# Optimization experiments

Measured on AMD Instinct MI355X. Metric: run time of the kernel, lower is better.

## Reference

```python
import jax, jax.numpy as jnp
import numpy as np

N_LEAVES = 32768
DEPTH = 16               # tree levels, leaves at level 0
N_NODES = 2 * N_LEAVES - 1
H = 256                  # h_size
X = 300                  # x_size
FEAT = 1024              # image feature_size
R = 49                   # image regions
VOCAB = 30000
CLASSES = 5


def setup_inputs() -> dict:
    ks = jax.random.split(jax.random.key(0), 10)
    wordid = jax.random.randint(ks[0], (N_NODES,), 0, VOCAB, dtype=jnp.int32)
    # leaves carry word tokens (mask=1), internal nodes don't (mask=0)
    mask = jnp.concatenate([jnp.ones(N_LEAVES, jnp.int32),
                            jnp.zeros(N_NODES - N_LEAVES, jnp.int32)])
    image = jax.random.normal(ks[1], (R, FEAT), dtype=jnp.float32)
    h0 = jnp.zeros((N_NODES, H), jnp.float32)
    c0 = jnp.zeros((N_NODES, H), jnp.float32)
    s = lambda k, shp, fan: jax.random.normal(k, shp, dtype=jnp.float32) * (1.0 / np.sqrt(fan))
    emb = s(ks[2], (VOCAB, X), X)
    attn_w_in = s(ks[3], (X, FEAT), FEAT)            # Attention.linear_in (no bias)
    attn_w_out = s(ks[4], (X, X + FEAT), X + FEAT)   # Attention.linear_out
    attn_b_out = jnp.zeros((X,), jnp.float32)
    w_iou = s(ks[5], (3 * H, X), X)                  # cell.W_iou (no bias)
    u_iou = s(ks[6], (3 * H, 2 * H), 2 * H)          # cell.U_iou (no bias)
    b_iou = jnp.zeros((1, 3 * H), jnp.float32)
    u_f_w = s(ks[7], (2 * H, 2 * H), 2 * H)          # cell.U_f
    u_f_b = jnp.zeros((2 * H,), jnp.float32)
    lin_w = s(ks[8], (CLASSES, H), H)                # final classifier
    lin_b = jnp.zeros((CLASSES,), jnp.float32)
    return dict(wordid=wordid, mask=mask, image=image, h0=h0, c0=c0, emb=emb,
                attn_w_in=attn_w_in, attn_w_out=attn_w_out, attn_b_out=attn_b_out,
                w_iou=w_iou, u_iou=u_iou, b_iou=b_iou, u_f_w=u_f_w, u_f_b=u_f_b,
                lin_w=lin_w, lin_b=lin_b)


def _forward(wordid, mask, image, h0, c0, emb, attn_w_in, attn_w_out, attn_b_out,
             w_iou, u_iou, b_iou, u_f_w, u_f_b, lin_w, lin_b):
    # --- embedding + attention over image regions ---
    embeds = emb[wordid * mask]                                  # [N, X]
    img_in = image @ attn_w_in.T                                 # [R, X]
    atten = jax.nn.softmax(embeds @ img_in.T, axis=1)            # [N, R]
    context = atten @ image                                      # [N, FEAT]
    sent = jnp.tanh(jnp.concatenate([context, embeds], axis=1) @ attn_w_out.T + attn_b_out)
    iou_x = (sent @ w_iou.T) * mask[:, None].astype(sent.dtype)  # [N, 3H] (dropout p=0 -> identity)

    def apply_node(iou, c_in):
        i, o, u = jnp.split(iou + b_iou, 3, axis=1)
        c_new = jax.nn.sigmoid(i) * jnp.tanh(u) + c_in
        return jax.nn.sigmoid(o) * jnp.tanh(c_new), c_new

    # --- leaves: no mailbox, apply_node with initial c ---
    h_leaf, c_leaf = apply_node(iou_x[:N_LEAVES], c0[:N_LEAVES])
    h = h0.at[:N_LEAVES].set(h_leaf)
    c = c0.at[:N_LEAVES].set(c_leaf)

    # --- topological propagation, one dense level at a time ---
    off_prev, sz, off = 0, N_LEAVES, N_LEAVES
    for _ in range(DEPTH - 1):
        sz_new = sz // 2
        h_cat = jax.lax.dynamic_slice_in_dim(h, off_prev, sz).reshape(sz_new, 2 * H)
        c_ch = jax.lax.dynamic_slice_in_dim(c, off_prev, sz).reshape(sz_new, 2, H)
        f = jax.nn.sigmoid(h_cat @ u_f_w.T + u_f_b).reshape(sz_new, 2, H)
        c_red = jnp.sum(f * c_ch, axis=1)                        # [sz_new, H]
        iou = h_cat @ u_iou.T                                    # reduce_func overwrites node iou
        h_new, c_new = apply_node(iou, c_red)
        h = h.at[off:off + sz_new].set(h_new)
        c = c.at[off:off + sz_new].set(c_new)
        off_prev, sz, off = off, sz_new, off + sz_new

    return h @ lin_w.T + lin_b                                   # [N, CLASSES]


def reference(wordid, mask, image, h0, c0, emb, attn_w_in, attn_w_out, attn_b_out,
              w_iou, u_iou, b_iou, u_f_w, u_f_b, lin_w, lin_b):
    return _forward(wordid, mask, image, h0, c0, emb, attn_w_in, attn_w_out, attn_b_out,
                    w_iou, u_iou, b_iou, u_f_w, u_f_b, lin_w, lin_b)
```

## Files before the change

### kernel.cpp

```cpp
#include <hip/hip_runtime.h>
#include <hip/hip_bf16.h>
#include <math.h>

#define N_LEAVES 32768
#define N_NODES  65535
#define DEPTH    16
#define H        256
#define XS       300
#define FEAT     1024
#define RR       49
#define CLASSES  5

#define XP 320
#define CATW 384

typedef __attribute__((ext_vector_type(8))) short bf16x8;
typedef __attribute__((ext_vector_type(4))) float f32x4;

__device__ __forceinline__ ushort f2bf(float v) {
    __hip_bfloat16 h = __float2bfloat16(v);
    return *reinterpret_cast<ushort*>(&h);
}
__device__ __forceinline__ float bf2f(ushort u) {
    __hip_bfloat16 h; *reinterpret_cast<ushort*>(&h) = u;
    return __bfloat162float(h);
}

__device__ __forceinline__ float fsig(float x) {
    float e = __builtin_amdgcn_exp2f(-1.44269504f * x);
    return __builtin_amdgcn_rcpf(1.0f + e);
}
__device__ __forceinline__ float ftanh(float x) {
    float xx = fmaxf(x, -20.0f);
    float e = __builtin_amdgcn_exp2f(-2.88539008f * xx);
    return (1.0f - e) * __builtin_amdgcn_rcpf(1.0f + e);
}
__device__ __forceinline__ float fexp(float x) {
    return __builtin_amdgcn_exp2f(1.44269504f * x);
}

__device__ __forceinline__ void swz_mj(int& mblk, int& jg) {
    int lid = blockIdx.y * gridDim.x + blockIdx.x;
    int mcount = gridDim.y, njg = gridDim.x;
    if ((mcount & 7) == 0) {
        int xcd = lid & 7, q = lid >> 3;
        jg = q % njg;
        mblk = xcd * (mcount >> 3) + q / njg;
    } else { mblk = blockIdx.y; jg = blockIdx.x; }
}

__device__ __forceinline__ ushort* lds_at(ushort* base, int row, int kbyte) {
    int off = row * 128 + kbyte;
    off ^= ((row & 7) << 4);
    return (ushort*)((char*)base + off);
}

__device__ __forceinline__ void gll16(const void* g, void* l) {
    __builtin_amdgcn_global_load_lds(
        (const __attribute__((address_space(1))) unsigned int*)g,
        (__attribute__((address_space(3))) unsigned int*)l, 16, 0, 0);
}

__device__ __forceinline__ void issue_tileA(const ushort* A, long lda, long m0, long mmax,
                                            int k0, ushort* buf, int R, int w, int lane)
{
    const int insts = R >> 5;
#pragma unroll
    for (int q = 0; q < 4; ++q) {
        if (q >= insts) break;
        int dest = (w * insts + q) * 1024;
        int row = (dest >> 7) + (lane >> 3);
        int kb = ((lane & 7) << 4) ^ ((row & 7) << 4);
        long am = m0 + row; if (am > mmax) am = mmax;
        gll16((const char*)(A + am * lda + k0) + kb, (char*)buf + dest);
    }
}

__global__ __launch_bounds__(256)
void k_sent(const ushort* __restrict__ A, const ushort* __restrict__ Wf,
            const float* __restrict__ bias, ushort* __restrict__ Cbf)
{
    __shared__ ushort At[2][128 * 64];
    const int tid = threadIdx.x;
    const int l = tid & 63;
    const int w = tid >> 6;
    const int wr = w >> 1, wc = w & 1;
    int mblk, nb; swz_mj(mblk, nb);
    const long m0 = (long)mblk * 128;
    const ushort* wb = Wf + (long)(nb * 2 + wc) * 6 * 8 * 512 + l * 8;

    bf16x8 wreg[2][4];
    f32x4 acc[4][4] = {};

    auto loadW = [&](int t) {
        const ushort* wt = wb + (long)t * 8 * 512;
#pragma unroll
        for (int kk = 0; kk < 2; ++kk)
#pragma unroll
            for (int j = 0; j < 4; ++j)
                wreg[kk][j] = *(const bf16x8*)(wt + (long)(kk * 4 + j) * 512);
    };

    issue_tileA(A, CATW, m0, N_LEAVES - 1, 0, At[0], 128, w, l);
    loadW(0);
    __syncthreads();
    for (int t = 0; t < 6; ++t) {
        ushort* Ab = At[t & 1];
#pragma unroll
        for (int kk = 0; kk < 2; ++kk) {
            bf16x8 af[4];
#pragma unroll
            for (int i = 0; i < 4; ++i)
                af[i] = *(const bf16x8*)lds_at(Ab, wr * 64 + i * 16 + (l & 15), kk * 64 + (l >> 4) * 16);
#pragma unroll
            for (int j = 0; j < 4; ++j)
#pragma unroll
                for (int i = 0; i < 4; ++i)
                    acc[i][j] = __builtin_amdgcn_mfma_f32_16x16x32_bf16(af[i], wreg[kk][j], acc[i][j], 0, 0, 0);
        }
        if (t + 1 < 6) {
            issue_tileA(A, CATW, m0, N_LEAVES - 1, (t + 1) * 64, At[(t + 1) & 1], 128, w, l);
            loadW(t + 1);
        }
        __syncthreads();
    }
#pragma unroll
    for (int i = 0; i < 4; ++i)
#pragma unroll
        for (int j = 0; j < 4; ++j)
#pragma unroll
            for (int r = 0; r < 4; ++r) {
                long m = m0 + wr * 64 + i * 16 + (l >> 4) * 4 + r;
                long n = (long)nb * 128 + wc * 64 + j * 16 + (l & 15);
                if (n < XS)
                    Cbf[m * XP + n] = f2bf(ftanh(acc[i][j][r] + bias[n]));
            }
}

__global__ __launch_bounds__(256)
void k_attn(const float* __restrict__ emb, const int* __restrict__ wid,
            const ushort* __restrict__ img, ushort* __restrict__ cat)
{
    __shared__ ushort At[128 * 64];
    __shared__ ushort Bt[64 * 64];
    const int tid = threadIdx.x;
    const int l = tid & 63;
    const int w = tid >> 6;
    const long m0 = (long)blockIdx.x * 128;
    const int srow = tid >> 3, skg = tid & 7;

    int wrd[4];
#pragma unroll
    for (int q = 0; q < 4; ++q) wrd[q] = wid[m0 + q * 32 + srow];

    float av[4][8];
    bf16x8 breg[2];
    f32x4 acc[2][4] = {};

    auto loadAB = [&](int t) {
        int c = t * 64 + skg * 8;
#pragma unroll
        for (int q = 0; q < 4; ++q) {
            const float* er = emb + (long)wrd[q] * XS;
            if (c + 8 <= XS) {
                float4 a = *(const float4*)(er + c);
                float4 b = *(const float4*)(er + c + 4);
                av[q][0] = a.x; av[q][1] = a.y; av[q][2] = a.z; av[q][3] = a.w;
                av[q][4] = b.x; av[q][5] = b.y; av[q][6] = b.z; av[q][7] = b.w;
            } else {
#pragma unroll
                for (int u = 0; u < 8; ++u) av[q][u] = (c + u < XS) ? er[c + u] : 0.f;
            }
        }
#pragma unroll
        for (int q = 0; q < 2; ++q)
            breg[q] = *(const bf16x8*)(img + (long)(q * 32 + srow) * XP + t * 64 + skg * 8);
    };
    auto writeAB = [&](int t) {
        int c = t * 64 + skg * 8;
#pragma unroll
        for (int q = 0; q < 4; ++q) {
            int row = q * 32 + srow;
            bf16x8 pk;
#pragma unroll
            for (int u = 0; u < 8; ++u) pk[u] = (short)f2bf(av[q][u]);
            *(bf16x8*)lds_at(At, row, skg * 16) = pk;
            *(bf16x8*)(cat + (m0 + row) * CATW + 64 + c) = pk;
        }
#pragma unroll
        for (int q = 0; q < 2; ++q)
            *(bf16x8*)lds_at(Bt, q * 32 + srow, skg * 16) = breg[q];
    };

    loadAB(0);
    writeAB(0);
    for (int t = 0; t < 5; ++t) {
        __syncthreads();
        if (t + 1 < 5) loadAB(t + 1);
#pragma unroll
        for (int kk = 0; kk < 2; ++kk) {
            bf16x8 af[2], bg[4];
#pragma unroll
            for (int i = 0; i < 2; ++i)
                af[i] = *(const bf16x8*)lds_at(At, w * 32 + i * 16 + (l & 15), kk * 64 + (l >> 4) * 16);
#pragma unroll
            for (int j = 0; j < 4; ++j)
                bg[j] = *(const bf16x8*)lds_at(Bt, j * 16 + (l & 15), kk * 64 + (l >> 4) * 16);
#pragma unroll
            for (int i = 0; i < 2; ++i)
#pragma unroll
                for (int j = 0; j < 4; ++j)
                    acc[i][j] = __builtin_amdgcn_mfma_f32_16x16x32_bf16(af[i], bg[j], acc[i][j], 0, 0, 0);
        }
        if (t + 1 < 5) {
            __syncthreads();
            writeAB(t + 1);
        }
    }
#pragma unroll
    for (int i = 0; i < 2; ++i)
#pragma unroll
        for (int r = 0; r < 4; ++r) {
            long m = m0 + w * 32 + i * 16 + (l >> 4) * 4 + r;
            float v[4]; float mx = -1e30f;
#pragma unroll
            for (int j = 0; j < 4; ++j) {
                int n = j * 16 + (l & 15);
                v[j] = (n < RR) ? acc[i][j][r] : -1e30f;
                mx = fmaxf(mx, v[j]);
            }
#pragma unroll
            for (int sh = 1; sh < 16; sh <<= 1) mx = fmaxf(mx, __shfl_xor(mx, sh));
            float e[4], s = 0.f;
#pragma unroll
            for (int j = 0; j < 4; ++j) { e[j] = fexp(v[j] - mx); s += e[j]; }
#pragma unroll
            for (int sh = 1; sh < 16; sh <<= 1) s += __shfl_xor(s, sh);
            float inv = __builtin_amdgcn_rcpf(s);
#pragma unroll
            for (int j = 0; j < 4; ++j)
                cat[m * CATW + j * 16 + (l & 15)] = f2bf(e[j] * inv);
        }
}

__global__ __launch_bounds__(256)
void k_leaf_fused(const ushort* __restrict__ A, const ushort* __restrict__ Wf,
                  const float* __restrict__ b_iou,
                  ushort* __restrict__ h, ushort* __restrict__ c)
{
    __shared__ ushort At[2][128 * 64];
    const int tid = threadIdx.x;
    const int l = tid & 63;
    const int w = tid >> 6;
    const int wr = w >> 1, wc = w & 1;
    int mblk, jg; swz_mj(mblk, jg);
    const long m0 = (long)mblk * 128;
    const ushort* wb = Wf + (long)(jg * 2 + wc) * 5 * 12 * 512 + l * 8;

    bf16x8 wreg[2][3][2];
    f32x4 acc[3][4][2] = {};

    auto loadW = [&](int t) {
        const ushort* wt = wb + (long)t * 12 * 512;
#pragma unroll
        for (int kk = 0; kk < 2; ++kk)
#pragma unroll
            for (int g = 0; g < 3; ++g)
#pragma unroll
                for (int j = 0; j < 2; ++j)
                    wreg[kk][g][j] = *(const bf16x8*)(wt + (long)((kk * 3 + g) * 2 + j) * 512);
    };

    issue_tileA(A, XP, m0, N_LEAVES - 1, 0, At[0], 128, w, l);
    loadW(0);
    __syncthreads();
    for (int t = 0; t < 5; ++t) {
        ushort* Ab = At[t & 1];
#pragma unroll
        for (int kk = 0; kk < 2; ++kk) {
            bf16x8 af[4];
#pragma unroll
            for (int i = 0; i < 4; ++i)
                af[i] = *(const bf16x8*)lds_at(Ab, wr * 64 + i * 16 + (l & 15), kk * 64 + (l >> 4) * 16);
#pragma unroll
            for (int g = 0; g < 3; ++g)
#pragma unroll
                for (int j = 0; j < 2; ++j)
#pragma unroll
                    for (int i = 0; i < 4; ++i)
                        acc[g][i][j] = __builtin_amdgcn_mfma_f32_16x16x32_bf16(af[i], wreg[kk][g][j], acc[g][i][j], 0, 0, 0);
        }
        if (t + 1 < 5) {
            issue_tileA(A, XP, m0, N_LEAVES - 1, (t + 1) * 64, At[(t + 1) & 1], 128, w, l);
            loadW(t + 1);
        }
        __syncthreads();
    }
#pragma unroll
    for (int i = 0; i < 4; ++i)
#pragma unroll
        for (int j = 0; j < 2; ++j) {
            int jglob = jg * 64 + wc * 32 + j * 16 + (l & 15);
            float bi = b_iou[jglob], bu = b_iou[512 + jglob], bo = b_iou[256 + jglob];
#pragma unroll
            for (int r = 0; r < 4; ++r) {
                long m = m0 + wr * 64 + i * 16 + (l >> 4) * 4 + r;
                float cn = fsig(acc[0][i][j][r] + bi) * ftanh(acc[1][i][j][r] + bu);
                c[m * H + jglob] = f2bf(cn);
                h[m * H + jglob] = f2bf(fsig(acc[2][i][j][r] + bo) * ftanh(cn));
            }
        }
}

__global__ __launch_bounds__(256)
void k_tree_fused(const ushort* __restrict__ A, const ushort* __restrict__ Wf,
                  const float* __restrict__ u_f_b, const float* __restrict__ b_iou,
                  const ushort* __restrict__ csrc,
                  ushort* __restrict__ hdst, ushort* __restrict__ cdst, int sz_new)
{
    __shared__ ushort At[2][64 * 64];
    const int tid = threadIdx.x;
    const int l = tid & 63;
    const int w = tid >> 6;
    const int wr = w >> 1, wc = w & 1;
    int mblk, jg; swz_mj(mblk, jg);
    const long m0 = (long)mblk * 64;
    const ushort* wb = Wf + (long)(jg * 2 + wc) * 8 * 20 * 512 + l * 8;

    bf16x8 wreg[2][5][2];
    f32x4 acc[5][2][2] = {};

    auto loadW = [&](int t) {
        const ushort* wt = wb + (long)t * 20 * 512;
#pragma unroll
        for (int kk = 0; kk < 2; ++kk)
#pragma unroll
            for (int g = 0; g < 5; ++g)
#pragma unroll
                for (int j = 0; j < 2; ++j)
                    wreg[kk][g][j] = *(const bf16x8*)(wt + (long)((kk * 5 + g) * 2 + j) * 512);
    };

    issue_tileA(A, 512, m0, sz_new - 1, 0, At[0], 64, w, l);
    loadW(0);
    __syncthreads();
    for (int t = 0; t < 8; ++t) {
        ushort* Ab = At[t & 1];
#pragma unroll
        for (int kk = 0; kk < 2; ++kk) {
            bf16x8 af[2];
#pragma unroll
            for (int i = 0; i < 2; ++i)
                af[i] = *(const bf16x8*)lds_at(Ab, wr * 32 + i * 16 + (l & 15), kk * 64 + (l >> 4) * 16);
#pragma unroll
            for (int g = 0; g < 5; ++g)
#pragma unroll
                for (int j = 0; j < 2; ++j)
#pragma unroll
                    for (int i = 0; i < 2; ++i)
                        acc[g][i][j] = __builtin_amdgcn_mfma_f32_16x16x32_bf16(af[i], wreg[kk][g][j], acc[g][i][j], 0, 0, 0);
        }
        if (t + 1 < 8) {
            issue_tileA(A, 512, m0, sz_new - 1, (t + 1) * 64, At[(t + 1) & 1], 64, w, l);
            loadW(t + 1);
        }
        __syncthreads();
    }
#pragma unroll
    for (int i = 0; i < 2; ++i)
#pragma unroll
        for (int j = 0; j < 2; ++j) {
            int jglob = jg * 64 + wc * 32 + j * 16 + (l & 15);
            float bf0 = u_f_b[jglob], bf1 = u_f_b[256 + jglob];
            float bi = b_iou[jglob], bu = b_iou[512 + jglob], bo = b_iou[256 + jglob];
#pragma unroll
            for (int r = 0; r < 4; ++r) {
                long m = m0 + wr * 32 + i * 16 + (l >> 4) * 4 + r;
                if (m < sz_new) {
                    float cl = bf2f(csrc[(2 * m) * H + jglob]);
                    float cr = bf2f(csrc[(2 * m + 1) * H + jglob]);
                    float S = fsig(acc[0][i][j][r] + bf0) * cl
                            + fsig(acc[1][i][j][r] + bf1) * cr;
                    float cn = fsig(acc[2][i][j][r] + bi) * ftanh(acc[3][i][j][r] + bu) + S;
                    cdst[m * H + jglob] = f2bf(cn);
                    hdst[m * H + jglob] = f2bf(fsig(acc[4][i][j][r] + bo) * ftanh(cn));
                }
            }
        }
}

__global__ __launch_bounds__(256)
void k_prep(const float* __restrict__ image, const float* __restrict__ w_in,
            const float* __restrict__ w_out, ushort* __restrict__ img_bf,
            ushort* __restrict__ wcat)
{
    const int wave = (blockIdx.x * 256 + threadIdx.x) >> 6;
    const int lane = threadIdx.x & 63;
    const int half = RR * XS;
    if (wave >= 2 * half) return;
    const float* wr; const float* ir; ushort* outp;
    if (wave < half) {
        int r = wave / XS, x = wave % XS;
        ir = image + (long)r * FEAT;
        wr = w_in + (long)x * FEAT;
        outp = img_bf + (long)r * XP + x;
    } else {
        int w2 = wave - half;
        int x = w2 / RR, r = w2 % RR;
        ir = image + (long)r * FEAT;
        wr = w_out + (long)x * (FEAT + XS);
        outp = wcat + (long)x * CATW + r;
    }
    float s = 0.f;
#pragma unroll
    for (int u = 0; u < FEAT / 64; ++u) {
        int f = lane + u * 64;
        s = fmaf(ir[f], wr[f], s);
    }
#pragma unroll
    for (int sh = 32; sh; sh >>= 1) s += __shfl_xor(s, sh);
    if (lane == 0) *outp = f2bf(s);
}

__global__ __launch_bounds__(256)
void k_cvt(ushort* __restrict__ dst, long dld, long doff,
           const float* __restrict__ src, long sld, long soff,
           int rows, int cols)
{
    long idx = (long)blockIdx.x * 256 + threadIdx.x;
    if (idx >= (long)rows * cols) return;
    int r = (int)(idx / cols), c = (int)(idx % cols);
    dst[r * dld + doff + c] = f2bf(src[r * sld + soff + c]);
}

__global__ __launch_bounds__(256)
void k_bld_wcatf(ushort* __restrict__ dst, const ushort* __restrict__ wcat)
{
    long idx = (long)blockIdx.x * 256 + threadIdx.x;
    if (idx >= 147456) return;
    int u = idx & 7; long r = idx >> 3;
    int l = r & 63; r >>= 6;
    int j = r & 3; r >>= 2;
    int kk = r & 1; r >>= 1;
    int t = (int)(r % 6); r /= 6;
    int wc = r & 1; r >>= 1;
    int nb = (int)r;
    int row = nb * 128 + wc * 64 + j * 16 + (l & 15);
    int col = t * 64 + kk * 32 + (l >> 4) * 8 + u;
    dst[idx] = wcat[(long)row * CATW + col];
}

__global__ __launch_bounds__(256)
void k_bld_w3f(ushort* __restrict__ dst, const float* __restrict__ w_iou)
{
    long idx = (long)blockIdx.x * 256 + threadIdx.x;
    if (idx >= 245760) return;
    int u = idx & 7; long r = idx >> 3;
    int l = r & 63; r >>= 6;
    int j = r & 1; r >>= 1;
    int g = (int)(r % 3); r /= 3;
    int kk = r & 1; r >>= 1;
    int t = (int)(r % 5); r /= 5;
    int wc = r & 1; r >>= 1;
    int jg = (int)r;
    int row = jg * 64 + wc * 32 + j * 16 + (l & 15);
    int col = t * 64 + kk * 32 + (l >> 4) * 8 + u;
    int srow = (g == 0) ? row : (g == 1) ? 512 + row : 256 + row;
    dst[idx] = (col < XS) ? f2bf(w_iou[(long)srow * XS + col]) : 0;
}

__global__ __launch_bounds__(256)
void k_bld_w5f(ushort* __restrict__ dst, const float* __restrict__ u_f_w,
               const float* __restrict__ u_iou)
{
    long idx = (long)blockIdx.x * 256 + threadIdx.x;
    if (idx >= 655360) return;
    int u = idx & 7; long r = idx >> 3;
    int l = r & 63; r >>= 6;
    int j = r & 1; r >>= 1;
    int g = (int)(r % 5); r /= 5;
    int kk = r & 1; r >>= 1;
    int t = (int)(r & 7); r >>= 3;
    int wc = r & 1; r >>= 1;
    int jg = (int)r;
    int row = jg * 64 + wc * 32 + j * 16 + (l & 15);
    int col = t * 64 + kk * 32 + (l >> 4) * 8 + u;
    const float* src;
    if (g == 0)      src = u_f_w + (long)row * 512;
    else if (g == 1) src = u_f_w + (long)(256 + row) * 512;
    else if (g == 2) src = u_iou + (long)row * 512;
    else if (g == 3) src = u_iou + (long)(512 + row) * 512;
    else             src = u_iou + (long)(256 + row) * 512;
    dst[idx] = f2bf(src[col]);
}

__global__ __launch_bounds__(256)
void k_classify(const ushort* __restrict__ h, const float* __restrict__ lin_w,
                const float* __restrict__ lin_b, float* __restrict__ out, int n_rows)
{
    const int node = (int)((blockIdx.x * 256 + threadIdx.x) >> 6);
    const int lane = threadIdx.x & 63;
    if (node >= n_rows) return;
    const ushort* hr = h + (long)node * H;
    float p[CLASSES] = {0.f};
#pragma unroll
    for (int u = 0; u < H / 64; ++u) {
        int j = lane + u * 64;
        float hv = bf2f(hr[j]);
#pragma unroll
        for (int cc = 0; cc < CLASSES; ++cc)
            p[cc] = fmaf(hv, lin_w[cc * H + j], p[cc]);
    }
#pragma unroll
    for (int cc = 0; cc < CLASSES; ++cc)
#pragma unroll
        for (int sh = 32; sh; sh >>= 1) p[cc] += __shfl_xor(p[cc], sh);
    if (lane == 0) {
#pragma unroll
        for (int cc = 0; cc < CLASSES; ++cc)
            out[(long)node * CLASSES + cc] = p[cc] + lin_b[cc];
    }
}

extern "C" void kernel_launch(void* const* d_in, const int* in_sizes, int n_in,
                              void* d_out, int out_size, void* d_ws, size_t ws_size,
                              hipStream_t stream)
{
    const int*   wordid     = (const int*)  d_in[0];
    const float* image      = (const float*)d_in[2];
    const float* emb        = (const float*)d_in[5];
    const float* attn_w_in  = (const float*)d_in[6];
    const float* attn_w_out = (const float*)d_in[7];
    const float* attn_b_out = (const float*)d_in[8];
    const float* w_iou      = (const float*)d_in[9];
    const float* u_iou      = (const float*)d_in[10];
    const float* b_iou      = (const float*)d_in[11];
    const float* u_f_w      = (const float*)d_in[12];
    const float* u_f_b      = (const float*)d_in[13];
    const float* lin_w      = (const float*)d_in[14];
    const float* lin_b      = (const float*)d_in[15];
    float* out = (float*)d_out;

    char* p = (char*)d_ws;
    auto alloc = [&](size_t bytes) { char* r = p; p += (bytes + 255) & ~255UL; return r; };
    ushort* cat     = (ushort*)alloc((size_t)N_LEAVES * CATW * 2);
    ushort* sentbf  = (ushort*)alloc((size_t)N_LEAVES * XP * 2);
    ushort* hall    = (ushort*)alloc((size_t)65536 * H * 2);
    ushort* cA      = (ushort*)alloc((size_t)N_LEAVES * H * 2);
    ushort* cB      = (ushort*)alloc((size_t)(N_LEAVES/2) * H * 2);
    ushort* img_bf  = (ushort*)alloc((size_t)64 * XP * 2);
    ushort* wcat    = (ushort*)alloc((size_t)CATW * CATW * 2);
    ushort* wcatf   = (ushort*)alloc((size_t)147456 * 2);
    ushort* w3f     = (ushort*)alloc((size_t)245760 * 2);
    ushort* w5f     = (ushort*)alloc((size_t)655360 * 2);
    (void)ws_size;

    hipMemsetAsync(img_bf, 0, (size_t)64 * XP * 2, stream);
    hipMemsetAsync(wcat,   0, (size_t)CATW * CATW * 2, stream);
    {
        int waves = 2 * RR * XS;
        k_prep<<<(waves * 64 + 255) / 256, 256, 0, stream>>>(image, attn_w_in,
                                                             attn_w_out, img_bf, wcat);
    }
    k_cvt<<<((long)XS * XS + 255) / 256, 256, 0, stream>>>(
        wcat, CATW, 64, attn_w_out, FEAT + XS, FEAT, XS, XS);
    k_bld_wcatf<<<(147456 + 255) / 256, 256, 0, stream>>>(wcatf, wcat);
    k_bld_w3f<<<(245760 + 255) / 256, 256, 0, stream>>>(w3f, w_iou);
    k_bld_w5f<<<(655360 + 255) / 256, 256, 0, stream>>>(w5f, u_f_w, u_iou);

    k_attn<<<N_LEAVES / 128, 256, 0, stream>>>(emb, wordid, img_bf, cat);
    k_sent<<<dim3(3, N_LEAVES / 128), 256, 0, stream>>>(cat, wcatf, attn_b_out, sentbf);
    k_leaf_fused<<<dim3(4, N_LEAVES / 128), 256, 0, stream>>>(
        sentbf, w3f, b_iou, hall, cA);

    ushort* csrc = cA; ushort* cdst = cB;
    int node_off = N_LEAVES;
    int sz = N_LEAVES;
    int off_prev = 0;
    for (int lvl = 0; lvl < DEPTH - 1; ++lvl) {
        int sz_new = sz / 2;
        k_tree_fused<<<dim3(4, (sz_new + 63) / 64), 256, 0, stream>>>(
            hall + (long)off_prev * H, w5f, u_f_b, b_iou, csrc,
            hall + (long)node_off * H, cdst, sz_new);
        off_prev = node_off;
        node_off += sz_new;
        ushort* t = csrc; csrc = cdst; cdst = t;
        sz = sz_new;
    }

    k_classify<<<((long)N_NODES * 64 + 255) / 256, 256, 0, stream>>>(
        hall, lin_w, lin_b, out, N_NODES);
}
```

Before: 349.0 us.

## Triple-buffer A tiles and split waves along N in MFMA GEMM kernels

Three GEMM kernels (sentence projection, leaf cell, internal-node cell) now use a three-stage LDS ring for A tiles, issued two steps ahead, and double-buffered weight registers. Each block now needs only one barrier per k-step. The wave layout changes from a 2x2 M/N grid to four waves that each cover the full M tile and a quarter of N, and the weight pre-packing kernels are rewritten to match. The goal is to hide global-load latency and cut synchronisation. The cost is more LDS, more A-fragment reads from LDS per wave, and higher register pressure.

```diff
diff --git a/kernel.cpp b/kernel.cpp
--- a/kernel.cpp
+++ b/kernel.cpp
@@ -39,6 +39,9 @@
     return __builtin_amdgcn_exp2f(1.44269504f * x);
 }
 
+#define SPIN() __builtin_amdgcn_sched_barrier(0)
+#define SBAR() { __builtin_amdgcn_s_barrier(); __builtin_amdgcn_sched_barrier(0); }
+
 __device__ __forceinline__ void swz_mj(int& mblk, int& jg) {
     int lid = blockIdx.y * gridDim.x + blockIdx.x;
     int mcount = gridDim.y, njg = gridDim.x;
@@ -80,61 +83,64 @@
 void k_sent(const ushort* __restrict__ A, const ushort* __restrict__ Wf,
             const float* __restrict__ bias, ushort* __restrict__ Cbf)
 {
-    __shared__ ushort At[2][128 * 64];
+    __shared__ ushort At[3][128 * 64];
     const int tid = threadIdx.x;
     const int l = tid & 63;
     const int w = tid >> 6;
-    const int wr = w >> 1, wc = w & 1;
     int mblk, nb; swz_mj(mblk, nb);
     const long m0 = (long)mblk * 128;
-    const ushort* wb = Wf + (long)(nb * 2 + wc) * 6 * 8 * 512 + l * 8;
-
-    bf16x8 wreg[2][4];
-    f32x4 acc[4][4] = {};
-
-    auto loadW = [&](int t) {
-        const ushort* wt = wb + (long)t * 8 * 512;
+    const ushort* wb = Wf + (size_t)(nb * 4 + w) * 24 * 512 + l * 8;
+
+    bf16x8 wreg[2][2][2];
+    f32x4 acc[2][8] = {};
+
+    auto loadW = [&](int t, int buf) {
+        const ushort* wt = wb + (long)t * 4 * 512;
 #pragma unroll
         for (int kk = 0; kk < 2; ++kk)
 #pragma unroll
-            for (int j = 0; j < 4; ++j)
-                wreg[kk][j] = *(const bf16x8*)(wt + (long)(kk * 4 + j) * 512);
+            for (int j = 0; j < 2; ++j)
+                wreg[buf][kk][j] = *(const bf16x8*)(wt + (long)(kk * 2 + j) * 512);
     };
 
     issue_tileA(A, CATW, m0, N_LEAVES - 1, 0, At[0], 128, w, l);
-    loadW(0);
     __syncthreads();
+    issue_tileA(A, CATW, m0, N_LEAVES - 1, 64, At[1], 128, w, l);
+    SPIN();
+    loadW(0, 0);
+#pragma unroll
     for (int t = 0; t < 6; ++t) {
-        ushort* Ab = At[t & 1];
+        if (t + 2 < 6) issue_tileA(A, CATW, m0, N_LEAVES - 1, (t + 2) * 64, At[(t + 2) % 3], 128, w, l);
+        SPIN();
+        if (t + 1 < 6) loadW(t + 1, (t + 1) & 1);
+        ushort* Ab = At[t % 3];
 #pragma unroll
         for (int kk = 0; kk < 2; ++kk) {
-            bf16x8 af[4];
-#pragma unroll
-            for (int i = 0; i < 4; ++i)
-                af[i] = *(const bf16x8*)lds_at(Ab, wr * 64 + i * 16 + (l & 15), kk * 64 + (l >> 4) * 16);
-#pragma unroll
-            for (int j = 0; j < 4; ++j)
-#pragma unroll
-                for (int i = 0; i < 4; ++i)
-                    acc[i][j] = __builtin_amdgcn_mfma_f32_16x16x32_bf16(af[i], wreg[kk][j], acc[i][j], 0, 0, 0);
-        }
-        if (t + 1 < 6) {
-            issue_tileA(A, CATW, m0, N_LEAVES - 1, (t + 1) * 64, At[(t + 1) & 1], 128, w, l);
-            loadW(t + 1);
-        }
-        __syncthreads();
-    }
-#pragma unroll
-    for (int i = 0; i < 4; ++i)
-#pragma unroll
-        for (int j = 0; j < 4; ++j)
+            bf16x8 af[8];
+#pragma unroll
+            for (int i = 0; i < 8; ++i)
+                af[i] = *(const bf16x8*)lds_at(Ab, i * 16 + (l & 15), kk * 64 + (l >> 4) * 16);
+#pragma unroll
+            for (int j = 0; j < 2; ++j)
+#pragma unroll
+                for (int i = 0; i < 8; ++i)
+                    acc[j][i] = __builtin_amdgcn_mfma_f32_16x16x32_bf16(af[i], wreg[t & 1][kk][j], acc[j][i], 0, 0, 0);
+        }
+        if (t + 1 < 6) SBAR();
+    }
+#pragma unroll
+    for (int j = 0; j < 2; ++j) {
+        long n = (long)nb * 128 + w * 32 + j * 16 + (l & 15);
+        if (n >= XS) continue;
+        float bn = bias[n];
+#pragma unroll
+        for (int i = 0; i < 8; ++i)
 #pragma unroll
             for (int r = 0; r < 4; ++r) {
-                long m = m0 + wr * 64 + i * 16 + (l >> 4) * 4 + r;
-                long n = (long)nb * 128 + wc * 64 + j * 16 + (l & 15);
-                if (n < XS)
-                    Cbf[m * XP + n] = f2bf(ftanh(acc[i][j][r] + bias[n]));
+                long m = m0 + i * 16 + (l >> 4) * 4 + r;
+                Cbf[m * XP + n] = f2bf(ftanh(acc[j][i][r] + bn));
             }
+    }
 }
 
 __global__ __launch_bounds__(256)
@@ -248,68 +254,64 @@
                   const float* __restrict__ b_iou,
                   ushort* __restrict__ h, ushort* __restrict__ c)
 {
-    __shared__ ushort At[2][128 * 64];
+    __shared__ ushort At[3][128 * 64];
     const int tid = threadIdx.x;
     const int l = tid & 63;
     const int w = tid >> 6;
-    const int wr = w >> 1, wc = w & 1;
     int mblk, jg; swz_mj(mblk, jg);
     const long m0 = (long)mblk * 128;
-    const ushort* wb = Wf + (long)(jg * 2 + wc) * 5 * 12 * 512 + l * 8;
-
-    bf16x8 wreg[2][3][2];
-    f32x4 acc[3][4][2] = {};
-
-    auto loadW = [&](int t) {
-        const ushort* wt = wb + (long)t * 12 * 512;
+    const ushort* wb = Wf + (size_t)(jg * 4 + w) * 30 * 512 + l * 8;
+
+    bf16x8 wreg[2][2][3];
+    f32x4 acc[3][8] = {};
+
+    auto loadW = [&](int t, int buf) {
+        const ushort* wt = wb + (long)t * 6 * 512;
 #pragma unroll
         for (int kk = 0; kk < 2; ++kk)
 #pragma unroll
             for (int g = 0; g < 3; ++g)
-#pragma unroll
-                for (int j = 0; j < 2; ++j)
-                    wreg[kk][g][j] = *(const bf16x8*)(wt + (long)((kk * 3 + g) * 2 + j) * 512);
+                wreg[buf][kk][g] = *(const bf16x8*)(wt + (long)(kk * 3 + g) * 512);
     };
 
     issue_tileA(A, XP, m0, N_LEAVES - 1, 0, At[0], 128, w, l);
-    loadW(0);
     __syncthreads();
+    issue_tileA(A, XP, m0, N_LEAVES - 1, 64, At[1], 128, w, l);
+    SPIN();
+    loadW(0, 0);
+#pragma unroll
     for (int t = 0; t < 5; ++t) {
-        ushort* Ab = At[t & 1];
+        if (t + 2 < 5) issue_tileA(A, XP, m0, N_LEAVES - 1, (t + 2) * 64, At[(t + 2) % 3], 128, w, l);
+        SPIN();
+        if (t + 1 < 5) loadW(t + 1, (t + 1) & 1);
+        ushort* Ab = At[t % 3];
 #pragma unroll
         for (int kk = 0; kk < 2; ++kk) {
-            bf16x8 af[4];
-#pragma unroll
-            for (int i = 0; i < 4; ++i)
-                af[i] = *(const bf16x8*)lds_at(Ab, wr * 64 + i * 16 + (l & 15), kk * 64 + (l >> 4) * 16);
+            bf16x8 af[8];
+#pragma unroll
+            for (int i = 0; i < 8; ++i)
+                af[i] = *(const bf16x8*)lds_at(Ab, i * 16 + (l & 15), kk * 64 + (l >> 4) * 16);
 #pragma unroll
             for (int g = 0; g < 3; ++g)
 #pragma unroll
-                for (int j = 0; j < 2; ++j)
-#pragma unroll
-                    for (int i = 0; i < 4; ++i)
-                        acc[g][i][j] = __builtin_amdgcn_mfma_f32_16x16x32_bf16(af[i], wreg[kk][g][j], acc[g][i][j], 0, 0, 0);
-        }
-        if (t + 1 < 5) {
-            issue_tileA(A, XP, m0, N_LEAVES - 1, (t + 1) * 64, At[(t + 1) & 1], 128, w, l);
-            loadW(t + 1);
-        }
-        __syncthreads();
-    }
-#pragma unroll
-    for (int i = 0; i < 4; ++i)
-#pragma unroll
-        for (int j = 0; j < 2; ++j) {
-            int jglob = jg * 64 + wc * 32 + j * 16 + (l & 15);
-            float bi = b_iou[jglob], bu = b_iou[512 + jglob], bo = b_iou[256 + jglob];
+                for (int i = 0; i < 8; ++i)
+                    acc[g][i] = __builtin_amdgcn_mfma_f32_16x16x32_bf16(af[i], wreg[t & 1][kk][g], acc[g][i], 0, 0, 0);
+        }
+        if (t + 1 < 5) SBAR();
+    }
+    {
+        int jglob = jg * 64 + w * 16 + (l & 15);
+        float bi = b_iou[jglob], bu = b_iou[512 + jglob], bo = b_iou[256 + jglob];
+#pragma unroll
+        for (int i = 0; i < 8; ++i)
 #pragma unroll
             for (int r = 0; r < 4; ++r) {
-                long m = m0 + wr * 64 + i * 16 + (l >> 4) * 4 + r;
-                float cn = fsig(acc[0][i][j][r] + bi) * ftanh(acc[1][i][j][r] + bu);
+                long m = m0 + i * 16 + (l >> 4) * 4 + r;
+                float cn = fsig(acc[0][i][r] + bi) * ftanh(acc[1][i][r] + bu);
                 c[m * H + jglob] = f2bf(cn);
-                h[m * H + jglob] = f2bf(fsig(acc[2][i][j][r] + bo) * ftanh(cn));
+                h[m * H + jglob] = f2bf(fsig(acc[2][i][r] + bo) * ftanh(cn));
             }
-        }
+    }
 }
 
 __global__ __launch_bounds__(256)
@@ -318,75 +320,71 @@
                   const ushort* __restrict__ csrc,
                   ushort* __restrict__ hdst, ushort* __restrict__ cdst, int sz_new)
 {
-    __shared__ ushort At[2][64 * 64];
+    __shared__ ushort At[3][64 * 64];
     const int tid = threadIdx.x;
     const int l = tid & 63;
     const int w = tid >> 6;
-    const int wr = w >> 1, wc = w & 1;
     int mblk, jg; swz_mj(mblk, jg);
     const long m0 = (long)mblk * 64;
-    const ushort* wb = Wf + (long)(jg * 2 + wc) * 8 * 20 * 512 + l * 8;
-
-    bf16x8 wreg[2][5][2];
-    f32x4 acc[5][2][2] = {};
-
-    auto loadW = [&](int t) {
-        const ushort* wt = wb + (long)t * 20 * 512;
+    const ushort* wb = Wf + (size_t)(jg * 4 + w) * 80 * 512 + l * 8;
+
+    bf16x8 wreg[2][2][5];
+    f32x4 acc[5][4] = {};
+
+    auto loadW = [&](int t, int buf) {
+        const ushort* wt = wb + (long)t * 10 * 512;
 #pragma unroll
         for (int kk = 0; kk < 2; ++kk)
 #pragma unroll
             for (int g = 0; g < 5; ++g)
-#pragma unroll
-                for (int j = 0; j < 2; ++j)
-                    wreg[kk][g][j] = *(const bf16x8*)(wt + (long)((kk * 5 + g) * 2 + j) * 512);
+                wreg[buf][kk][g] = *(const bf16x8*)(wt + (long)(kk * 5 + g) * 512);
     };
 
     issue_tileA(A, 512, m0, sz_new - 1, 0, At[0], 64, w, l);
-    loadW(0);
     __syncthreads();
+    issue_tileA(A, 512, m0, sz_new - 1, 64, At[1], 64, w, l);
+    SPIN();
+    loadW(0, 0);
+#pragma unroll
     for (int t = 0; t < 8; ++t) {
-        ushort* Ab = At[t & 1];
+        if (t + 2 < 8) issue_tileA(A, 512, m0, sz_new - 1, (t + 2) * 64, At[(t + 2) % 3], 64, w, l);
+        SPIN();
+        if (t + 1 < 8) loadW(t + 1, (t + 1) & 1);
+        ushort* Ab = At[t % 3];
 #pragma unroll
         for (int kk = 0; kk < 2; ++kk) {
-            bf16x8 af[2];
-#pragma unroll
-            for (int i = 0; i < 2; ++i)
-                af[i] = *(const bf16x8*)lds_at(Ab, wr * 32 + i * 16 + (l & 15), kk * 64 + (l >> 4) * 16);
+            bf16x8 af[4];
+#pragma unroll
+            for (int i = 0; i < 4; ++i)
+                af[i] = *(const bf16x8*)lds_at(Ab, i * 16 + (l & 15), kk * 64 + (l >> 4) * 16);
 #pragma unroll
             for (int g = 0; g < 5; ++g)
 #pragma unroll
-                for (int j = 0; j < 2; ++j)
-#pragma unroll
-                    for (int i = 0; i < 2; ++i)
-                        acc[g][i][j] = __builtin_amdgcn_mfma_f32_16x16x32_bf16(af[i], wreg[kk][g][j], acc[g][i][j], 0, 0, 0);
-        }
-        if (t + 1 < 8) {
-            issue_tileA(A, 512, m0, sz_new - 1, (t + 1) * 64, At[(t + 1) & 1], 64, w, l);
-            loadW(t + 1);
-        }
-        __syncthreads();
-    }
-#pragma unroll
-    for (int i = 0; i < 2; ++i)
-#pragma unroll
-        for (int j = 0; j < 2; ++j) {
-            int jglob = jg * 64 + wc * 32 + j * 16 + (l & 15);
-            float bf0 = u_f_b[jglob], bf1 = u_f_b[256 + jglob];
-            float bi = b_iou[jglob], bu = b_iou[512 + jglob], bo = b_iou[256 + jglob];
+                for (int i = 0; i < 4; ++i)
+                    acc[g][i] = __builtin_amdgcn_mfma_f32_16x16x32_bf16(af[i], wreg[t & 1][kk][g], acc[g][i], 0, 0, 0);
+        }
+        if (t + 1 < 8) SBAR();
+    }
+    {
+        int jglob = jg * 64 + w * 16 + (l & 15);
+        float bf0 = u_f_b[jglob], bf1 = u_f_b[256 + jglob];
+        float bi = b_iou[jglob], bu = b_iou[512 + jglob], bo = b_iou[256 + jglob];
+#pragma unroll
+        for (int i = 0; i < 4; ++i)
 #pragma unroll
             for (int r = 0; r < 4; ++r) {
-                long m = m0 + wr * 32 + i * 16 + (l >> 4) * 4 + r;
+                long m = m0 + i * 16 + (l >> 4) * 4 + r;
                 if (m < sz_new) {
                     float cl = bf2f(csrc[(2 * m) * H + jglob]);
                     float cr = bf2f(csrc[(2 * m + 1) * H + jglob]);
-                    float S = fsig(acc[0][i][j][r] + bf0) * cl
-                            + fsig(acc[1][i][j][r] + bf1) * cr;
-                    float cn = fsig(acc[2][i][j][r] + bi) * ftanh(acc[3][i][j][r] + bu) + S;
+                    float S = fsig(acc[0][i][r] + bf0) * cl
+                            + fsig(acc[1][i][r] + bf1) * cr;
+                    float cn = fsig(acc[2][i][r] + bi) * ftanh(acc[3][i][r] + bu) + S;
                     cdst[m * H + jglob] = f2bf(cn);
-                    hdst[m * H + jglob] = f2bf(fsig(acc[4][i][j][r] + bo) * ftanh(cn));
+                    hdst[m * H + jglob] = f2bf(fsig(acc[4][i][r] + bo) * ftanh(cn));
                 }
             }
-        }
+    }
 }
 
 __global__ __launch_bounds__(256)
@@ -440,12 +438,12 @@
     if (idx >= 147456) return;
     int u = idx & 7; long r = idx >> 3;
     int l = r & 63; r >>= 6;
-    int j = r & 3; r >>= 2;
+    int j = r & 1; r >>= 1;
     int kk = r & 1; r >>= 1;
     int t = (int)(r % 6); r /= 6;
-    int wc = r & 1; r >>= 1;
+    int wq = r & 3; r >>= 2;
     int nb = (int)r;
-    int row = nb * 128 + wc * 64 + j * 16 + (l & 15);
+    int row = nb * 128 + wq * 32 + j * 16 + (l & 15);
     int col = t * 64 + kk * 32 + (l >> 4) * 8 + u;
     dst[idx] = wcat[(long)row * CATW + col];
 }
@@ -457,13 +455,12 @@
     if (idx >= 245760) return;
     int u = idx & 7; long r = idx >> 3;
     int l = r & 63; r >>= 6;
-    int j = r & 1; r >>= 1;
     int g = (int)(r % 3); r /= 3;
     int kk = r & 1; r >>= 1;
     int t = (int)(r % 5); r /= 5;
-    int wc = r & 1; r >>= 1;
+    int wq = r & 3; r >>= 2;
     int jg = (int)r;
-    int row = jg * 64 + wc * 32 + j * 16 + (l & 15);
+    int row = jg * 64 + wq * 16 + (l & 15);
     int col = t * 64 + kk * 32 + (l >> 4) * 8 + u;
     int srow = (g == 0) ? row : (g == 1) ? 512 + row : 256 + row;
     dst[idx] = (col < XS) ? f2bf(w_iou[(long)srow * XS + col]) : 0;
@@ -477,13 +474,12 @@
     if (idx >= 655360) return;
     int u = idx & 7; long r = idx >> 3;
     int l = r & 63; r >>= 6;
-    int j = r & 1; r >>= 1;
     int g = (int)(r % 5); r /= 5;
     int kk = r & 1; r >>= 1;
     int t = (int)(r & 7); r >>= 3;
-    int wc = r & 1; r >>= 1;
+    int wq = r & 3; r >>= 2;
     int jg = (int)r;
-    int row = jg * 64 + wc * 32 + j * 16 + (l & 15);
+    int row = jg * 64 + wq * 16 + (l & 15);
     int col = t * 64 + kk * 32 + (l >> 4) * 8 + u;
     const float* src;
     if (g == 0)      src = u_f_w + (long)row * 512;
```

Measured after the change: 315.4 us. -9.6%, faster.
